# Performance work log

Measured on AMD Instinct MI355X. Metric: run time of the kernel, lower is better.

The kernel has to match this reference:

```python
import jax, jax.numpy as jnp
import numpy as np


def setup_inputs() -> dict:
    key = jax.random.key(0)
    ks = jax.random.split(key, 6)
    B, H, W, Cin, Cout, wdim = 8, 64, 64, 512, 512, 512
    return {
        "x": jax.random.normal(ks[0], (B, H, W, Cin), jnp.float32),
        "w": jax.random.normal(ks[1], (B, wdim), jnp.float32),
        "noise": jax.random.normal(ks[2], (B, H, W, 1), jnp.float32),
        "style_weight": jax.random.normal(ks[3], (wdim, Cin), jnp.float32),
        "style_bias": jnp.ones((Cin,), jnp.float32),
        "conv_weight": jax.random.normal(ks[4], (3, 3, Cin, Cout), jnp.float32),
        "scale_noise": 0.1 * jax.random.normal(ks[5], (1, 1, 1, Cout), jnp.float32),
        "bias": jax.random.normal(jax.random.fold_in(key, 7), (Cout,), jnp.float32),
    }


def reference(x, w, noise, style_weight, style_bias, conv_weight, scale_noise, bias):
    wdim = style_weight.shape[0]
    kh, kw, cin, cout = conv_weight.shape
    # Equalized-LR fully connected to_style (gain=1, lr_mult=1, bias init ones,
    # activation=True -> leaky_relu(0.2) with sqrt(2) gain, StyleGAN2 convention).
    s = w @ (style_weight * (1.0 / np.sqrt(wdim))) + style_bias  # [B, Cin]
    s = jax.nn.leaky_relu(s, 0.2) * np.sqrt(2.0).astype(np.float32)
    # Modulated conv (demodulated). Equalized-LR weight scale 1/sqrt(fan_in).
    wk = conv_weight * (1.0 / np.sqrt(kh * kw * cin))  # [3,3,Cin,Cout]
    # demod[b,o] = rsqrt(sum_{h,w,i} (wk[h,w,i,o]*s[b,i])^2 + eps)
    d = jax.lax.rsqrt(jnp.einsum('hwio,bi->bo', wk * wk, s * s) + 1e-8)  # [B,Cout]
    xm = x * s[:, None, None, :]  # modulate inputs instead of per-sample weights
    y = jax.lax.conv_general_dilated(
        xm, wk, window_strides=(1, 1), padding='SAME',
        dimension_numbers=('NHWC', 'HWIO', 'NHWC'))
    y = y * d[:, None, None, :]
    # noise scale-add + bias + leaky-relu (the fused tail in StyleGAN2 kernels)
    y = y + scale_noise * noise + bias
    return jax.nn.leaky_relu(y, 0.2)
```

## Files before the change

kernel.cpp:

```cpp
#include <hip/hip_runtime.h>
#include <hip/hip_bf16.h>
#include <stdint.h>


typedef __attribute__((ext_vector_type(8))) __bf16 bf16x8;
typedef __attribute__((ext_vector_type(16))) float f32x16;

__device__ __forceinline__ float bf2f(ushort u) {
    union { uint32_t i; float f; } v; v.i = (uint32_t)u << 16; return v.f;
}
__device__ __forceinline__ ushort f2bf(float f) {
    union { float f; uint32_t i; } v; v.f = f;
    uint32_t r = v.i + 0x7fffu + ((v.i >> 16) & 1u);
    return (ushort)(r >> 16);
}
__device__ __forceinline__ int sniff_f32(const void* sb) {
    return ((const uint32_t*)sb)[0] == 0x3F800000u;
}
__device__ __forceinline__ float lda(const void* p, int idx, int isf) {
    return isf ? ((const float*)p)[idx] : bf2f(((const ushort*)p)[idx]);
}

union U16x8 { uint4 v; ushort u[8]; };

#define INV_SQRT_WDIM 0.04419417382415922f
#define SQRT2         1.4142135623730951f
#define WSCALE        0.014731391274719739f

__global__ void k_style_part(const void* __restrict__ w, const void* __restrict__ sw,
                             const void* __restrict__ sb, float* __restrict__ part) {
    int isf = sniff_f32(sb);
    int b = blockIdx.x >> 3, ds = blockIdx.x & 7;
    int i = threadIdx.x;
    __shared__ float wrow[64];
    if (i < 64) wrow[i] = lda(w, b * 512 + ds * 64 + i, isf);
    __syncthreads();
    float acc = 0.f;
    if (isf) {
        const float* p = (const float*)sw + (size_t)ds * 64 * 512;
#pragma unroll 8
        for (int d = 0; d < 64; ++d) acc += wrow[d] * p[d * 512 + i];
    } else {
        const ushort* p = (const ushort*)sw + (size_t)ds * 64 * 512;
#pragma unroll 8
        for (int d = 0; d < 64; ++d) acc += wrow[d] * bf2f(p[d * 512 + i]);
    }
    part[(b * 8 + ds) * 512 + i] = acc;
}

__device__ __forceinline__ float style_s(const float* __restrict__ spart,
                                         const void* __restrict__ sb,
                                         int b, int i, int isf) {
    float a = 0.f;
#pragma unroll
    for (int ds = 0; ds < 8; ++ds) a += spart[(b * 8 + ds) * 512 + i];
    float s = a * INV_SQRT_WDIM + lda(sb, i, isf);
    return (s > 0.f ? s : 0.2f * s) * SQRT2;
}

__global__ void k_prep(const void* __restrict__ cw, const void* __restrict__ x,
                       const float* __restrict__ spart, const void* __restrict__ sb,
                       ushort* __restrict__ wkt2, ushort* __restrict__ xmp2,
                       float* __restrict__ part) {
    int isf = sniff_f32(sb);
    int bid = blockIdx.x;
    int tid = threadIdx.x;
    __shared__ __align__(16) char pool[34816];

    if (bid < 576) {
        ushort (*smw)[512] = (ushort (*)[512])pool;
        int t = bid / 64, ckg = bid % 64;
#pragma unroll
        for (int r = 0; r < 16; ++r) {
            int l = r * 256 + tid;
            int j = l >> 9, o = l & 511;
            float v = lda(cw, (size_t)(t * 512 + ckg * 8 + j) * 512 + o, isf);
            smw[j][o] = f2bf(v * WSCALE);
        }
        __syncthreads();
#pragma unroll
        for (int r = 0; r < 2; ++r) {
            int o = r * 256 + tid;
            U16x8 pk;
#pragma unroll
            for (int j = 0; j < 8; ++j) pk.u[j] = smw[j][o];
            *(uint4*)(wkt2 + ((size_t)(t * 64 + ckg) * 512 + o) * 8) = pk.v;
        }
        return;
    }
    if (bid < 1104) {
        float* sv = (float*)pool;
        ushort* tr = (ushort*)(pool + 2048);
        int pr = bid - 576;
        int b = pr / 66, yp = pr % 66;
        ushort* xb2 = xmp2 + (size_t)b * 2230272;
        uint4 z = {0u, 0u, 0u, 0u};
        if (yp == 0 || yp == 65) {
            for (int l = tid; l < 4224; l += 256) {
                int h = l / 132, cc = l - h * 132;
                *(uint4*)(xb2 + (size_t)(h * 66 + yp) * 1056 + cc * 8) = z;
            }
            return;
        }
        for (int i = tid; i < 512; i += 256) sv[i] = style_s(spart, sb, b, i, isf);
        if (tid < 64) {
            int h = tid & 31, side = tid >> 5;
            ushort* op = xb2 + ((size_t)(h * 66 + yp) * 66 + side * 65) * 16;
            *(uint4*)(op) = z;
            *(uint4*)(op + 8) = z;
        }
        int y = yp - 1;
        __syncthreads();
#pragma unroll 1
        for (int p = 0; p < 2; ++p) {
            if (p) __syncthreads();
            int c0 = p * 32;
#pragma unroll
            for (int r = 0; r < 4; ++r) {
                int u = r * 256 + tid;
                int hg = u & 31, col = u >> 5;
                U16x8 o0_, o1_;
                const float* sp = sv + hg * 16;
                if (isf) {
                    const float* xin = (const float*)x
                        + (((size_t)(b * 64 + y)) * 64 + c0 + col) * 512 + hg * 16;
                    float4 f0 = *(const float4*)(xin + 0);
                    float4 f1 = *(const float4*)(xin + 4);
                    float4 f2 = *(const float4*)(xin + 8);
                    float4 f3 = *(const float4*)(xin + 12);
                    o0_.u[0] = f2bf(f0.x * sp[0]);  o0_.u[1] = f2bf(f0.y * sp[1]);
                    o0_.u[2] = f2bf(f0.z * sp[2]);  o0_.u[3] = f2bf(f0.w * sp[3]);
                    o0_.u[4] = f2bf(f1.x * sp[4]);  o0_.u[5] = f2bf(f1.y * sp[5]);
                    o0_.u[6] = f2bf(f1.z * sp[6]);  o0_.u[7] = f2bf(f1.w * sp[7]);
                    o1_.u[0] = f2bf(f2.x * sp[8]);  o1_.u[1] = f2bf(f2.y * sp[9]);
                    o1_.u[2] = f2bf(f2.z * sp[10]); o1_.u[3] = f2bf(f2.w * sp[11]);
                    o1_.u[4] = f2bf(f3.x * sp[12]); o1_.u[5] = f2bf(f3.y * sp[13]);
                    o1_.u[6] = f2bf(f3.z * sp[14]); o1_.u[7] = f2bf(f3.w * sp[15]);
                } else {
                    const ushort* xin = (const ushort*)x
                        + (((size_t)(b * 64 + y)) * 64 + c0 + col) * 512 + hg * 16;
                    U16x8 i0, i1;
                    i0.v = *(const uint4*)(xin);
                    i1.v = *(const uint4*)(xin + 8);
#pragma unroll
                    for (int j = 0; j < 8; ++j) o0_.u[j] = f2bf(bf2f(i0.u[j]) * sp[j]);
#pragma unroll
                    for (int j = 0; j < 8; ++j) o1_.u[j] = f2bf(bf2f(i1.u[j]) * sp[8 + j]);
                }
                int cs = col ^ (hg & 7);
                *(uint4*)(tr + ((hg * 2 + 0) * 32 + cs) * 8) = o0_.v;
                *(uint4*)(tr + ((hg * 2 + 1) * 32 + cs) * 8) = o1_.v;
            }
            __syncthreads();
#pragma unroll
            for (int r = 0; r < 4; ++r) {
                int v = r * 256 + tid;
                int col = v & 31, hg = v >> 5;
                int cs = col ^ (hg & 7);
                uint4 a0 = *(const uint4*)(tr + ((hg * 2 + 0) * 32 + cs) * 8);
                uint4 a1 = *(const uint4*)(tr + ((hg * 2 + 1) * 32 + cs) * 8);
                ushort* op = xb2 + ((size_t)(hg * 66 + yp) * 66 + (c0 + col + 1)) * 16;
                *(uint4*)(op) = a0;
                *(uint4*)(op + 8) = a1;
            }
        }
        return;
    }
    {
        float* s2 = (float*)pool;
        float* red = (float*)(pool + 16384);
        int q2 = bid - 1104;
        int t = q2 / 8, ob = q2 % 8;
#pragma unroll
        for (int j = 0; j < 16; ++j) {
            int idx = j * 256 + tid;
            int bb = idx >> 9, i = idx & 511;
            float scv = style_s(spart, sb, bb, i, isf);
            s2[idx] = scv * scv;
        }
        __syncthreads();
        int q = tid >> 6, ol = tid & 63;
        int o = ob * 64 + ol;
        float accd[8] = {0, 0, 0, 0, 0, 0, 0, 0};
        for (int ii = 0; ii < 128; ++ii) {
            int i = q * 128 + ii;
            float wf = lda(cw, (size_t)(t * 512 + i) * 512 + o, isf) * WSCALE;
            float w2 = wf * wf;
#pragma unroll
            for (int bb = 0; bb < 8; ++bb) accd[bb] += w2 * s2[bb * 512 + i];
        }
#pragma unroll
        for (int bb = 0; bb < 8; ++bb) red[(ol * 8 + bb) * 4 + q] = accd[bb];
        __syncthreads();
#pragma unroll
        for (int p = 0; p < 2; ++p) {
            int u = tid * 2 + p;
            int ol2 = u >> 3, b2 = u & 7;
            float sum = red[u * 4 + 0] + red[u * 4 + 1] + red[u * 4 + 2] + red[u * 4 + 3];
            part[(b2 * 9 + t) * 512 + ob * 64 + ol2] = sum;
        }
    }
}

#define GLL(gp, lp) __builtin_amdgcn_global_load_lds( \
    (const __attribute__((address_space(1))) void*)(gp), \
    (__attribute__((address_space(3))) void*)(lp), 16, 0, 0)

__launch_bounds__(256, 2)
__global__ void k_conv(const ushort* __restrict__ xmp2, const ushort* __restrict__ wkt2,
                       const float* __restrict__ part, const void* __restrict__ noise,
                       const void* __restrict__ snoise, const void* __restrict__ bias_,
                       const void* __restrict__ sb, void* __restrict__ out) {
    __shared__ ushort Ah[2][6336];
    int isf = sniff_f32(sb);
    int id = blockIdx.x;
    int ct = id & 3;
    int rt = (id >> 2) & 15;
    int b  = id >> 6;
    int y0 = rt * 4, o0 = ct * 128;
    int tid = threadIdx.x;
    int lane = tid & 63, wv = tid >> 6;
    int wr = wv >> 1, wc = wv & 1;
    int lm = lane & 31, kh = lane >> 5;
    const ushort* xb2 = xmp2 + (size_t)b * 2230272;
    const ushort* wB = wkt2 + kh * 4096 + (size_t)(o0 + wc * 64 + lm) * 8;

    auto stageA = [&](int hp, int buf) {
        char* dst = (char*)Ah[buf];
#pragma unroll
        for (int it = 0; it < 3; ++it) {
            int L = it * 256 + tid;
            int hr = L / 132, rem = L - hr * 132;
            GLL(xb2 + (size_t)(hp * 66 + y0 + hr) * 1056 + rem * 8, dst + L * 16);
        }
        if (tid < 24) {
            int L = 768 + tid;
            int rem = L - 660;
            GLL(xb2 + (size_t)(hp * 66 + y0 + 5) * 1056 + rem * 8, dst + L * 16);
        }
    };
    auto loadB = [&](int t, int h, bf16x8 (&d)[2]) {
        const ushort* p = wB + (size_t)t * 262144 + h * 8192;
        d[0] = *(const bf16x8*)(p);
        d[1] = *(const bf16x8*)(p + 256);
    };

    f32x16 acc[4][2] = {};
    bf16x8 b0[2], b1[2], b2[2];

    stageA(0, 0);
    loadB(0, 0, b0);
    loadB(1, 0, b1);
    loadB(2, 0, b2);
    __syncthreads();

#pragma unroll 1
    for (int h = 0; h < 32; ++h) {
        const char* AhC = (const char*)Ah[h & 1];
        bf16x8 afA[4], afB[4];
        auto ldA = [&](int t, bf16x8 (&af)[4]) {
            int dy = t / 3 - 1, dx = t % 3 - 1;
#pragma unroll
            for (int am = 0; am < 4; ++am)
                af[am] = *(const bf16x8*)(AhC
                    + (wr * 2 + (am >> 1) + dy + 1) * 2112
                    + ((am & 1) * 32 + lm + dx + 1) * 32 + kh * 16);
        };
        auto mm = [&](const bf16x8 (&af)[4], const bf16x8 (&bf)[2]) {
            __builtin_amdgcn_s_setprio(1);
#pragma unroll
            for (int am = 0; am < 4; ++am)
#pragma unroll
                for (int bn = 0; bn < 2; ++bn)
                    acc[am][bn] = __builtin_amdgcn_mfma_f32_32x32x16_bf16(
                        af[am], bf[bn], acc[am][bn], 0, 0, 0);
            __builtin_amdgcn_s_setprio(0);
        };
        ldA(0, afA);
        ldA(1, afB); mm(afA, b0); loadB(3, h, b0);
        if (h < 31) stageA(h + 1, (h + 1) & 1);
        ldA(2, afA); mm(afB, b1); loadB(4, h, b1);
        ldA(3, afB); mm(afA, b2); loadB(5, h, b2);
        ldA(4, afA); mm(afB, b0); loadB(6, h, b0);
        ldA(5, afB); mm(afA, b1); loadB(7, h, b1);
        ldA(6, afA); mm(afB, b2); loadB(8, h, b2);
        ldA(7, afB); mm(afA, b0); if (h < 31) loadB(0, h + 1, b0);
        ldA(8, afA); mm(afB, b1); if (h < 31) loadB(1, h + 1, b1);
        mm(afA, b2);              if (h < 31) loadB(2, h + 1, b2);
        if (h < 31) __syncthreads();
    }

    float dv[2], snv[2], bv[2];
#pragma unroll
    for (int bn = 0; bn < 2; ++bn) {
        int o = o0 + wc * 64 + bn * 32 + lm;
        float a = 1e-8f;
#pragma unroll
        for (int t = 0; t < 9; ++t) a += part[(b * 9 + t) * 512 + o];
        dv[bn] = rsqrtf(a);
        snv[bn] = lda(snoise, o, isf);
        bv[bn] = lda(bias_, o, isf);
    }
#pragma unroll
    for (int am = 0; am < 4; ++am) {
#pragma unroll
        for (int reg = 0; reg < 16; ++reg) {
            int crow = 4 * kh + (reg & 3) + 8 * (reg >> 2);
            int yy = y0 + wr * 2 + (am >> 1);
            int xx = (am & 1) * 32 + crow;
            float nz = lda(noise, (b * 64 + yy) * 64 + xx, isf);
            size_t obase = ((size_t)(b * 64 + yy) * 64 + xx) * 512;
            if (isf) {
                float* of = (float*)out;
#pragma unroll
                for (int bn = 0; bn < 2; ++bn) {
                    float v = acc[am][bn][reg] * dv[bn] + snv[bn] * nz + bv[bn];
                    v = v > 0.f ? v : 0.2f * v;
                    of[obase + o0 + wc * 64 + bn * 32 + lm] = v;
                }
            } else {
                ushort* ob = (ushort*)out;
#pragma unroll
                for (int bn = 0; bn < 2; ++bn) {
                    float v = acc[am][bn][reg] * dv[bn] + snv[bn] * nz + bv[bn];
                    v = v > 0.f ? v : 0.2f * v;
                    ob[obase + o0 + wc * 64 + bn * 32 + lm] = f2bf(v);
                }
            }
        }
    }
}

extern "C" void kernel_launch(void* const* d_in, const int* in_sizes, int n_in,
                              void* d_out, int out_size, void* d_ws, size_t ws_size,
                              hipStream_t stream) {
    const void* x     = d_in[0];
    const void* w     = d_in[1];
    const void* noise = d_in[2];
    const void* sw    = d_in[3];
    const void* sb    = d_in[4];
    const void* cw    = d_in[5];
    const void* sn    = d_in[6];
    const void* bias  = d_in[7];

    char* ws = (char*)d_ws;
    ushort* xmp2  = (ushort*)(ws);
    ushort* wkt2  = (ushort*)(ws + 35684352);
    float*  part  = (float*)(ws + 40435712);
    float*  spart = (float*)(ws + 40583168);
    (void)in_sizes; (void)n_in; (void)out_size; (void)ws_size;

    hipLaunchKernelGGL(k_style_part, dim3(64),   dim3(512), 0, stream, w, sw, sb, spart);
    hipLaunchKernelGGL(k_prep,       dim3(1176), dim3(256), 0, stream,
                       cw, x, spart, sb, wkt2, xmp2, part);
    hipLaunchKernelGGL(k_conv,       dim3(512),  dim3(256), 0, stream,
                       xmp2, wkt2, part, noise, sn, bias, sb, d_out);
}
```

Measured before the change: 299.8 us.

## Split LDS A-tile by k-half plane and drop A-fragment double buffering

Reorganizes the staged input tile in LDS from interleaved 32-byte pixel records into two separate planes, one per 8-channel k-half. This should change the bank access pattern of the 16-byte fragment reads. It also removes the software-pipelined A-fragment ping-pong and the s_setprio hints, so each tap loads its fragments and then issues its MFMAs. The next-slice staging now starts after three taps instead of after the first. Dropping the explicit LDS/MFMA overlap could expose LDS latency unless the compiler schedules around it.

```diff
diff --git a/kernel.cpp b/kernel.cpp
--- a/kernel.cpp
+++ b/kernel.cpp
@@ -230,13 +230,17 @@
 #pragma unroll
         for (int it = 0; it < 3; ++it) {
             int L = it * 256 + tid;
-            int hr = L / 132, rem = L - hr * 132;
-            GLL(xb2 + (size_t)(hp * 66 + y0 + hr) * 1056 + rem * 8, dst + L * 16);
+            int ck2 = L / 396, rem = L - ck2 * 396;
+            int hr = rem / 66, col = rem - hr * 66;
+            GLL(xb2 + (size_t)(hp * 66 + y0 + hr) * 1056 + col * 16 + ck2 * 8,
+                dst + L * 16);
         }
         if (tid < 24) {
             int L = 768 + tid;
-            int rem = L - 660;
-            GLL(xb2 + (size_t)(hp * 66 + y0 + 5) * 1056 + rem * 8, dst + L * 16);
+            int rem = L - 396;
+            int col = rem - 330;
+            GLL(xb2 + (size_t)(hp * 66 + y0 + 5) * 1056 + col * 16 + 8,
+                dst + L * 16);
         }
     };
     auto loadB = [&](int t, int h, bf16x8 (&d)[2]) {
@@ -257,36 +261,32 @@
 #pragma unroll 1
     for (int h = 0; h < 32; ++h) {
         const char* AhC = (const char*)Ah[h & 1];
-        bf16x8 afA[4], afB[4];
-        auto ldA = [&](int t, bf16x8 (&af)[4]) {
+        auto tap = [&](int t, const bf16x8 (&bf)[2]) {
             int dy = t / 3 - 1, dx = t % 3 - 1;
+            bf16x8 afr[4];
 #pragma unroll
             for (int am = 0; am < 4; ++am)
-                af[am] = *(const bf16x8*)(AhC
-                    + (wr * 2 + (am >> 1) + dy + 1) * 2112
-                    + ((am & 1) * 32 + lm + dx + 1) * 32 + kh * 16);
-        };
-        auto mm = [&](const bf16x8 (&af)[4], const bf16x8 (&bf)[2]) {
-            __builtin_amdgcn_s_setprio(1);
+                afr[am] = *(const bf16x8*)(AhC
+                    + (kh * 396
+                       + (wr * 2 + (am >> 1) + dy + 1) * 66
+                       + ((am & 1) * 32 + lm + dx + 1)) * 16);
 #pragma unroll
             for (int am = 0; am < 4; ++am)
 #pragma unroll
                 for (int bn = 0; bn < 2; ++bn)
                     acc[am][bn] = __builtin_amdgcn_mfma_f32_32x32x16_bf16(
-                        af[am], bf[bn], acc[am][bn], 0, 0, 0);
-            __builtin_amdgcn_s_setprio(0);
+                        afr[am], bf[bn], acc[am][bn], 0, 0, 0);
         };
-        ldA(0, afA);
-        ldA(1, afB); mm(afA, b0); loadB(3, h, b0);
+        tap(0, b0); loadB(3, h, b0);
+        tap(1, b1); loadB(4, h, b1);
+        tap(2, b2); loadB(5, h, b2);
         if (h < 31) stageA(h + 1, (h + 1) & 1);
-        ldA(2, afA); mm(afB, b1); loadB(4, h, b1);
-        ldA(3, afB); mm(afA, b2); loadB(5, h, b2);
-        ldA(4, afA); mm(afB, b0); loadB(6, h, b0);
-        ldA(5, afB); mm(afA, b1); loadB(7, h, b1);
-        ldA(6, afA); mm(afB, b2); loadB(8, h, b2);
-        ldA(7, afB); mm(afA, b0); if (h < 31) loadB(0, h + 1, b0);
-        ldA(8, afA); mm(afB, b1); if (h < 31) loadB(1, h + 1, b1);
-        mm(afA, b2);              if (h < 31) loadB(2, h + 1, b2);
+        tap(3, b0); loadB(6, h, b0);
+        tap(4, b1); loadB(7, h, b1);
+        tap(5, b2); loadB(8, h, b2);
+        tap(6, b0); if (h < 31) loadB(0, h + 1, b0);
+        tap(7, b1); if (h < 31) loadB(1, h + 1, b1);
+        tap(8, b2); if (h < 31) loadB(2, h + 1, b2);
         if (h < 31) __syncthreads();
     }
 
```

New measurement: 306.0 us. 2.1% more time.
